# Kernel optimization log

Hardware: AMD Instinct MI355X
Metric: run time of the kernel (lower is better)

The kernel has to match this reference:

```python
import jax, jax.numpy as jnp
import numpy as np

EPS_LOG = 1e-20
EPS_DENOM = 1e-6
TEMP = 0.07  # temperature init; module uses exp(log(1/temp)) = 1/temp


def _log(t):
    return jnp.log(t + EPS_LOG)


def _masked_mean(t, mask, axis):
    t = jnp.where(mask, t, 0.0)
    numer = t.sum(axis=axis)
    denom = jnp.maximum(mask.sum(axis=axis).astype(t.dtype), EPS_DENOM)
    return numer / denom


def setup_inputs() -> dict:
    key = jax.random.key(0)
    k1, k2 = jax.random.split(key)
    B, T, I, D = 64, 64, 196, 512
    vision = jax.random.normal(k1, (B, I, D), dtype=jnp.float32)
    text = jax.random.normal(k2, (B, T, D), dtype=jnp.float32)
    # L2-normalize (as produced upstream in FILIP/CLIP) to keep exp(sim/temp) stable
    vision = vision / jnp.linalg.norm(vision, axis=-1, keepdims=True)
    text = text / jnp.linalg.norm(text, axis=-1, keepdims=True)
    vision_mask = jnp.ones((B, I), dtype=bool)
    text_mask = jnp.ones((B, T), dtype=bool)
    return {"vision": vision, "text": text, "vision_mask": vision_mask, "text_mask": text_mask}


def reference(vision, text, vision_mask, text_mask):
    temp = jnp.exp(jnp.log(jnp.asarray(1.0 / TEMP, dtype=text.dtype)))
    neg = -jnp.finfo(text.dtype).max
    # sim[x, y, t, i] = <text[x, t], vision[y, i]> * temp
    sim = jnp.einsum('xtd,yid->xyti', text, vision) * temp
    # text -> image: max over image tokens i (invalid patches masked out)
    t2i = jnp.where(vision_mask[None, :, None, :], sim, neg).max(axis=-1)  # [x, y, t]
    t2i = _masked_mean(t2i, text_mask[:, None, :], axis=-1)                # [x, y]
    # image -> text: max over text tokens t (invalid tokens masked out)
    i2t = jnp.where(text_mask[:, None, :, None], sim, neg).max(axis=-2)    # [x, y, i]
    i2t = _masked_mean(i2t, vision_mask[None, :, :], axis=-1)              # [x, y]
    t2i_exp = jnp.exp(t2i)
    i2t_exp = jnp.exp(i2t)
    t2i_pos = jnp.diagonal(t2i_exp)
    i2t_pos = jnp.diagonal(i2t_exp)
    t2i_denom = t2i_exp.sum(axis=-1)
    i2t_denom = i2t_exp.sum(axis=0)
    t2i_loss = (-_log(t2i_pos) + _log(t2i_denom)).mean(axis=-1)
    i2t_loss = (-_log(i2t_pos) + _log(i2t_denom)).mean(axis=-1)
    filip_loss = (t2i_loss + i2t_loss) / 2
    return (filip_loss, t2i_loss, i2t_loss)
```

## Files before the change

### kernel.cpp

```cpp
#include <hip/hip_runtime.h>
#include <cstdint>
#include <cstddef>

#define BATCH   64
#define TTOK    64
#define ITOK    196
#define NPAD    224
#define DDIM    512
#define BK      64
#define NTILE   (DDIM/BK)
#define XPB     4
#define MROWS   (XPB*TTOK)
#define TEMPINV 14.285714285714286f
#define EPS_LOG 1e-20f

typedef __bf16 bf16x8 __attribute__((ext_vector_type(8)));
typedef float  floatx4 __attribute__((ext_vector_type(4)));
typedef unsigned short ushort8 __attribute__((ext_vector_type(8)));

__device__ __forceinline__ void async_load16(const void* g, void* l) {
  __builtin_amdgcn_global_load_lds(
      (const __attribute__((address_space(1))) void*)g,
      (__attribute__((address_space(3))) void*)l, 16, 0, 0);
}

__device__ __forceinline__ unsigned short f2bf(float f) {
  unsigned int u = __float_as_uint(f);
  u += 0x7fffu + ((u >> 16) & 1u);
  return (unsigned short)(u >> 16);
}

#define NV_PAD (64*224*512)
#define NT_ALL (64*64*512)

__global__ void convert_kernel(const float* __restrict__ vis,
                               const float* __restrict__ txt,
                               unsigned short* __restrict__ visb,
                               unsigned short* __restrict__ txtb) {
  int t = blockIdx.x * 256 + threadIdx.x;
  int e = t * 8;
  if (e < NV_PAD) {
    int img = e / (NPAD * DDIM);
    int rem = e - img * (NPAD * DDIM);
    int row = rem >> 9;
    int d   = rem & 511;
    ushort8 o;
    if (row < ITOK) {
      const float4* src = (const float4*)(vis + ((size_t)img * ITOK + row) * DDIM + d);
      float4 a = src[0];
      float4 b = src[1];
      o[0] = f2bf(a.x); o[1] = f2bf(a.y); o[2] = f2bf(a.z); o[3] = f2bf(a.w);
      o[4] = f2bf(b.x); o[5] = f2bf(b.y); o[6] = f2bf(b.z); o[7] = f2bf(b.w);
    } else {
      o = (ushort8){0, 0, 0, 0, 0, 0, 0, 0};
    }
    *(ushort8*)(visb + e) = o;
  } else {
    int j = e - NV_PAD;
    const float4* src = (const float4*)(txt + j);
    float4 a = src[0];
    float4 b = src[1];
    ushort8 o;
    o[0] = f2bf(a.x); o[1] = f2bf(a.y); o[2] = f2bf(a.z); o[3] = f2bf(a.w);
    o[4] = f2bf(b.x); o[5] = f2bf(b.y); o[6] = f2bf(b.z); o[7] = f2bf(b.w);
    *(ushort8*)(txtb + j) = o;
  }
}

__global__ __launch_bounds__(512, 1) void filip_gemm(
    const unsigned short* __restrict__ txtb,
    const unsigned short* __restrict__ visb,
    float* __restrict__ T2I,
    float* __restrict__ I2T)
{
  __shared__ unsigned short As[2][MROWS * BK];
  __shared__ unsigned short Bs[2][NPAD * BK];
  __shared__ float t2i_part[MROWS][2];
  __shared__ float i2t_part[XPB][NPAD];

  const int tid  = threadIdx.x;
  const int lane = tid & 63;
  const int wave = tid >> 6;
  const int wm   = wave >> 1;
  const int wn   = wave & 1;
  const int lrow = lane & 15;
  const int lq   = lane >> 4;

  const int orig = blockIdx.x;
  const int xcd  = orig & 7;
  const int idx  = orig >> 3;
  const int y    = xcd * 8 + (idx & 7);
  const int xg   = idx >> 3;

  const unsigned short* tbase = txtb + (size_t)(xg * XPB) * (TTOK * DDIM);
  const unsigned short* vbase = visb + (size_t)y * (NPAD * DDIM);

  int aoff[4], boff[4];
#pragma unroll
  for (int r = 0; r < 4; ++r) {
    int s = r * 512 + tid;
    int row = s >> 3;
    int cg = (s & 7) ^ (row & 7);
    aoff[r] = row * DDIM + cg * 8;
  }
#pragma unroll
  for (int r = 0; r < 3; ++r) {
    int s = r * 512 + tid;
    int row = s >> 3;
    int cg = (s & 7) ^ (row & 7);
    boff[r] = row * DDIM + cg * 8;
  }
  {
    int s = 1536 + tid;
    int row = s >> 3;
    int cg = (s & 7) ^ (row & 7);
    boff[3] = (tid < 256) ? row * DDIM + cg * 8 : 0;
  }

  int bro0[7], bro1[7];
#pragma unroll
  for (int nt = 0; nt < 7; ++nt) {
    int row = wn * 112 + nt * 16 + lrow;
    bro0[nt] = row * BK + ((0 + lq) ^ (row & 7)) * 8;
    bro1[nt] = row * BK + ((4 + lq) ^ (row & 7)) * 8;
  }
  int aro0[4], aro1[4];
#pragma unroll
  for (int mt = 0; mt < 4; ++mt) {
    int row = wm * 64 + mt * 16 + lrow;
    aro0[mt] = row * BK + ((0 + lq) ^ (row & 7)) * 8;
    aro1[mt] = row * BK + ((4 + lq) ^ (row & 7)) * 8;
  }

  floatx4 acc[4][7];
#pragma unroll
  for (int mt = 0; mt < 4; ++mt)
#pragma unroll
    for (int nt = 0; nt < 7; ++nt)
      acc[mt][nt] = (floatx4){0.f, 0.f, 0.f, 0.f};

  {
#pragma unroll
    for (int r = 0; r < 4; ++r)
      async_load16(tbase + aoff[r], &As[0][(r * 512 + tid) * 8]);
#pragma unroll
    for (int r = 0; r < 3; ++r)
      async_load16(vbase + boff[r], &Bs[0][(r * 512 + tid) * 8]);
    if (tid < 256)
      async_load16(vbase + boff[3], &Bs[0][(1536 + tid) * 8]);
  }
  asm volatile("s_waitcnt vmcnt(0)" ::: "memory");
  __builtin_amdgcn_s_barrier();

  for (int t = 0; t < NTILE; ++t) {
    const int cur = t & 1;
    const int nxt = cur ^ 1;
    const int k1 = (t + 1) * BK;
    const bool pf = (t + 1 < NTILE);
    const unsigned short* Ac = &As[cur][0];
    const unsigned short* Bc = &Bs[cur][0];
    unsigned short* An = &As[nxt][0];
    unsigned short* Bn = &Bs[nxt][0];

    bf16x8 b0[7], b1[7], a00, a01, a02, a03, a10, a11, a12, a13;

    if (pf) {
      async_load16(tbase + aoff[0] + k1, An + (0 * 512 + tid) * 8);
      async_load16(tbase + aoff[1] + k1, An + (1 * 512 + tid) * 8);
      async_load16(tbase + aoff[2] + k1, An + (2 * 512 + tid) * 8);
    }
#pragma unroll
    for (int nt = 0; nt < 7; ++nt) b0[nt] = *(const bf16x8*)(Bc + bro0[nt]);
    a00 = *(const bf16x8*)(Ac + aro0[0]);
    a01 = *(const bf16x8*)(Ac + aro0[1]);
    __builtin_amdgcn_s_barrier();
    asm volatile("s_waitcnt lgkmcnt(0)" ::: "memory");
    __builtin_amdgcn_sched_barrier(0);
    __builtin_amdgcn_s_setprio(1);
#pragma unroll
    for (int nt = 0; nt < 7; ++nt) {
      acc[0][nt] = __builtin_amdgcn_mfma_f32_16x16x32_bf16(a00, b0[nt], acc[0][nt], 0, 0, 0);
      acc[1][nt] = __builtin_amdgcn_mfma_f32_16x16x32_bf16(a01, b0[nt], acc[1][nt], 0, 0, 0);
    }
    __builtin_amdgcn_s_setprio(0);
    __builtin_amdgcn_s_barrier();

    if (pf) {
      async_load16(tbase + aoff[3] + k1, An + (3 * 512 + tid) * 8);
      async_load16(vbase + boff[0] + k1, Bn + (0 * 512 + tid) * 8);
      async_load16(vbase + boff[1] + k1, Bn + (1 * 512 + tid) * 8);
    }
    a02 = *(const bf16x8*)(Ac + aro0[2]);
    a03 = *(const bf16x8*)(Ac + aro0[3]);
    __builtin_amdgcn_s_barrier();
    asm volatile("s_waitcnt lgkmcnt(0)" ::: "memory");
    __builtin_amdgcn_sched_barrier(0);
    __builtin_amdgcn_s_setprio(1);
#pragma unroll
    for (int nt = 0; nt < 7; ++nt) {
      acc[2][nt] = __builtin_amdgcn_mfma_f32_16x16x32_bf16(a02, b0[nt], acc[2][nt], 0, 0, 0);
      acc[3][nt] = __builtin_amdgcn_mfma_f32_16x16x32_bf16(a03, b0[nt], acc[3][nt], 0, 0, 0);
    }
    __builtin_amdgcn_s_setprio(0);
    __builtin_amdgcn_s_barrier();

    if (pf) {
      async_load16(vbase + boff[2] + k1, Bn + (2 * 512 + tid) * 8);
      if (tid < 256)
        async_load16(vbase + boff[3] + k1, Bn + (1536 + tid) * 8);
    }
#pragma unroll
    for (int nt = 0; nt < 7; ++nt) b1[nt] = *(const bf16x8*)(Bc + bro1[nt]);
    a10 = *(const bf16x8*)(Ac + aro1[0]);
    a11 = *(const bf16x8*)(Ac + aro1[1]);
    __builtin_amdgcn_s_barrier();
    asm volatile("s_waitcnt lgkmcnt(0)" ::: "memory");
    __builtin_amdgcn_sched_barrier(0);
    __builtin_amdgcn_s_setprio(1);
#pragma unroll
    for (int nt = 0; nt < 7; ++nt) {
      acc[0][nt] = __builtin_amdgcn_mfma_f32_16x16x32_bf16(a10, b1[nt], acc[0][nt], 0, 0, 0);
      acc[1][nt] = __builtin_amdgcn_mfma_f32_16x16x32_bf16(a11, b1[nt], acc[1][nt], 0, 0, 0);
    }
    __builtin_amdgcn_s_setprio(0);
    __builtin_amdgcn_s_barrier();

    a12 = *(const bf16x8*)(Ac + aro1[2]);
    a13 = *(const bf16x8*)(Ac + aro1[3]);
    __builtin_amdgcn_s_barrier();
    asm volatile("s_waitcnt lgkmcnt(0)" ::: "memory");
    __builtin_amdgcn_sched_barrier(0);
    __builtin_amdgcn_s_setprio(1);
#pragma unroll
    for (int nt = 0; nt < 7; ++nt) {
      acc[2][nt] = __builtin_amdgcn_mfma_f32_16x16x32_bf16(a12, b1[nt], acc[2][nt], 0, 0, 0);
      acc[3][nt] = __builtin_amdgcn_mfma_f32_16x16x32_bf16(a13, b1[nt], acc[3][nt], 0, 0, 0);
    }
    __builtin_amdgcn_s_setprio(0);
    asm volatile("s_waitcnt vmcnt(0)" ::: "memory");
    __builtin_amdgcn_s_barrier();
  }

#pragma unroll
  for (int mt = 0; mt < 4; ++mt) {
    float rm[4] = {-1e30f, -1e30f, -1e30f, -1e30f};
#pragma unroll
    for (int nt = 0; nt < 7; ++nt) {
      int col = wn * 112 + nt * 16 + lrow;
      if (col < ITOK) {
#pragma unroll
        for (int j = 0; j < 4; ++j) rm[j] = fmaxf(rm[j], acc[mt][nt][j]);
      }
    }
#pragma unroll
    for (int off = 1; off < 16; off <<= 1) {
#pragma unroll
      for (int j = 0; j < 4; ++j) rm[j] = fmaxf(rm[j], __shfl_xor(rm[j], off, 64));
    }
    if (lrow == 0) {
#pragma unroll
      for (int j = 0; j < 4; ++j)
        t2i_part[wm * 64 + mt * 16 + lq * 4 + j][wn] = rm[j];
    }
  }

#pragma unroll
  for (int nt = 0; nt < 7; ++nt) {
    float cm = -1e30f;
#pragma unroll
    for (int mt = 0; mt < 4; ++mt)
#pragma unroll
      for (int j = 0; j < 4; ++j) cm = fmaxf(cm, acc[mt][nt][j]);
    cm = fmaxf(cm, __shfl_xor(cm, 16, 64));
    cm = fmaxf(cm, __shfl_xor(cm, 32, 64));
    if (lq == 0) i2t_part[wm][wn * 112 + nt * 16 + lrow] = cm;
  }
  __syncthreads();

  if (wave < XPB) {
    const int p = wave;
    float ts = fmaxf(t2i_part[p * 64 + lane][0], t2i_part[p * 64 + lane][1]);
#pragma unroll
    for (int off = 32; off; off >>= 1) ts += __shfl_xor(ts, off, 64);
    float is = 0.f;
    for (int c = lane; c < ITOK; c += 64)
      is += i2t_part[p][c];
#pragma unroll
    for (int off = 32; off; off >>= 1) is += __shfl_xor(is, off, 64);
    if (lane == 0) {
      int o = (xg * XPB + p) * BATCH + y;
      T2I[o] = TEMPINV * ts * (1.0f / TTOK);
      I2T[o] = TEMPINV * is * (1.0f / ITOK);
    }
  }
}

__global__ void finalize_kernel(const float* __restrict__ T2I,
                                const float* __restrict__ I2T,
                                float* __restrict__ out) {
  int lane = threadIdx.x;
  float td = 0.f, idn = 0.f;
  for (int y = 0; y < BATCH; ++y) td  += expf(T2I[lane * BATCH + y]);
  for (int xx = 0; xx < BATCH; ++xx) idn += expf(I2T[xx * BATCH + lane]);
  float tpos = expf(T2I[lane * (BATCH + 1)]);
  float ipos = expf(I2T[lane * (BATCH + 1)]);
  float tl = -logf(tpos + EPS_LOG) + logf(td + EPS_LOG);
  float il = -logf(ipos + EPS_LOG) + logf(idn + EPS_LOG);
#pragma unroll
  for (int off = 32; off; off >>= 1) {
    tl += __shfl_xor(tl, off, 64);
    il += __shfl_xor(il, off, 64);
  }
  if (lane == 0) {
    float t2i_loss = tl * (1.0f / BATCH);
    float i2t_loss = il * (1.0f / BATCH);
    out[0] = 0.5f * (t2i_loss + i2t_loss);
    out[1] = t2i_loss;
    out[2] = i2t_loss;
  }
}

extern "C" void kernel_launch(void* const* d_in, const int* in_sizes, int n_in,
                              void* d_out, int out_size, void* d_ws, size_t ws_size,
                              hipStream_t stream) {
  const float* vis = (const float*)d_in[0];
  const float* txt = (const float*)d_in[1];
  float* out = (float*)d_out;

  char* ws = (char*)d_ws;
  unsigned short* visb = (unsigned short*)ws;
  unsigned short* txtb = (unsigned short*)(ws + (size_t)NV_PAD * 2);
  float* T2I = (float*)(ws + (size_t)(NV_PAD + NT_ALL) * 2);
  float* I2T = T2I + BATCH * BATCH;

  convert_kernel<<<(NV_PAD + NT_ALL) / 8 / 256, 256, 0, stream>>>(vis, txt, visb, txtb);
  filip_gemm<<<(BATCH / XPB) * BATCH, 512, 0, stream>>>(txtb, visb, T2I, I2T);
  finalize_kernel<<<1, 64, 0, stream>>>(T2I, I2T, out);
}
```

Before: 158.7 us.

## Split K tiles into half-stages with finer-grained async prefetch and waits

Restructures the GEMM staging so each 64-wide K tile is split into two 32-wide halves with separate LDS buffers. Prefetches are issued per half, and partial vmcnt waits let compute on the first half start before the second half lands. Vision padding grows to 256 rows so A and B share one uniform load pattern, which adds conversion and memory traffic for the padded rows. The finalize kernel is also parallelized across 256 threads, and the convert kernel's image indexing now uses shifts.

Result: faster. 153.5 us (-3.2%).

```diff
diff --git a/kernel.cpp b/kernel.cpp
--- a/kernel.cpp
+++ b/kernel.cpp
@@ -6,6 +6,7 @@
 #define TTOK    64
 #define ITOK    196
 #define NPAD    224
+#define VROWS   256
 #define DDIM    512
 #define BK      64
 #define NTILE   (DDIM/BK)
@@ -30,7 +31,7 @@
   return (unsigned short)(u >> 16);
 }
 
-#define NV_PAD (64*224*512)
+#define NV_PAD (64*VROWS*512)
 #define NT_ALL (64*64*512)
 
 __global__ void convert_kernel(const float* __restrict__ vis,
@@ -40,8 +41,8 @@
   int t = blockIdx.x * 256 + threadIdx.x;
   int e = t * 8;
   if (e < NV_PAD) {
-    int img = e / (NPAD * DDIM);
-    int rem = e - img * (NPAD * DDIM);
+    int img = e >> 17;
+    int rem = e & 131071;
     int row = rem >> 9;
     int d   = rem & 511;
     ushort8 o;
@@ -73,8 +74,8 @@
     float* __restrict__ T2I,
     float* __restrict__ I2T)
 {
-  __shared__ unsigned short As[2][MROWS * BK];
-  __shared__ unsigned short Bs[2][NPAD * BK];
+  __shared__ unsigned short As[2][2][VROWS * 32];
+  __shared__ unsigned short Bs[2][2][VROWS * 32];
   __shared__ float t2i_part[MROWS][2];
   __shared__ float i2t_part[XPB][NPAD];
 
@@ -93,43 +94,29 @@
   const int xg   = idx >> 3;
 
   const unsigned short* tbase = txtb + (size_t)(xg * XPB) * (TTOK * DDIM);
-  const unsigned short* vbase = visb + (size_t)y * (NPAD * DDIM);
-
-  int aoff[4], boff[4];
-#pragma unroll
-  for (int r = 0; r < 4; ++r) {
-    int s = r * 512 + tid;
-    int row = s >> 3;
-    int cg = (s & 7) ^ (row & 7);
-    aoff[r] = row * DDIM + cg * 8;
-  }
-#pragma unroll
-  for (int r = 0; r < 3; ++r) {
-    int s = r * 512 + tid;
-    int row = s >> 3;
-    int cg = (s & 7) ^ (row & 7);
-    boff[r] = row * DDIM + cg * 8;
-  }
-  {
-    int s = 1536 + tid;
-    int row = s >> 3;
-    int cg = (s & 7) ^ (row & 7);
-    boff[3] = (tid < 256) ? row * DDIM + cg * 8 : 0;
-  }
-
-  int bro0[7], bro1[7];
+  const unsigned short* vbase = visb + (size_t)y * (VROWS * DDIM);
+
+  int qoff[2];
+#pragma unroll
+  for (int r = 0; r < 2; ++r) {
+    int s  = r * 512 + tid;
+    int r2 = s >> 3;
+    int cg = (s & 7) ^ (r2 & 7);
+    qoff[r] = (2 * r2 + (cg >> 2)) * DDIM + (cg & 3) * 8;
+  }
+
+  int aro[4], bro[7];
+#pragma unroll
+  for (int mt = 0; mt < 4; ++mt) {
+    int row = wm * 64 + mt * 16 + lrow;
+    int r2  = row >> 1;
+    aro[mt] = r2 * 64 + (((((row & 1) << 2) + lq) ^ (r2 & 7)) << 3);
+  }
 #pragma unroll
   for (int nt = 0; nt < 7; ++nt) {
     int row = wn * 112 + nt * 16 + lrow;
-    bro0[nt] = row * BK + ((0 + lq) ^ (row & 7)) * 8;
-    bro1[nt] = row * BK + ((4 + lq) ^ (row & 7)) * 8;
-  }
-  int aro0[4], aro1[4];
-#pragma unroll
-  for (int mt = 0; mt < 4; ++mt) {
-    int row = wm * 64 + mt * 16 + lrow;
-    aro0[mt] = row * BK + ((0 + lq) ^ (row & 7)) * 8;
-    aro1[mt] = row * BK + ((4 + lq) ^ (row & 7)) * 8;
+    int r2  = row >> 1;
+    bro[nt] = r2 * 64 + (((((row & 1) << 2) + lq) ^ (r2 & 7)) << 3);
   }
 
   floatx4 acc[4][7];
@@ -139,17 +126,20 @@
     for (int nt = 0; nt < 7; ++nt)
       acc[mt][nt] = (floatx4){0.f, 0.f, 0.f, 0.f};
 
-  {
-#pragma unroll
-    for (int r = 0; r < 4; ++r)
-      async_load16(tbase + aoff[r], &As[0][(r * 512 + tid) * 8]);
-#pragma unroll
-    for (int r = 0; r < 3; ++r)
-      async_load16(vbase + boff[r], &Bs[0][(r * 512 + tid) * 8]);
-    if (tid < 256)
-      async_load16(vbase + boff[3], &Bs[0][(1536 + tid) * 8]);
-  }
-  asm volatile("s_waitcnt vmcnt(0)" ::: "memory");
+  auto stageAh = [&](int b, int h, int kbase) {
+    async_load16(tbase + qoff[0] + kbase, &As[b][h][(0 * 512 + tid) * 8]);
+    async_load16(tbase + qoff[1] + kbase, &As[b][h][(1 * 512 + tid) * 8]);
+  };
+  auto stageBh = [&](int b, int h, int kbase) {
+    async_load16(vbase + qoff[0] + kbase, &Bs[b][h][(0 * 512 + tid) * 8]);
+    async_load16(vbase + qoff[1] + kbase, &Bs[b][h][(1 * 512 + tid) * 8]);
+  };
+
+  stageAh(0, 0, 0);
+  stageBh(0, 0, 0);
+  stageAh(0, 1, 32);
+  stageBh(0, 1, 32);
+  asm volatile("s_waitcnt vmcnt(4)" ::: "memory");
   __builtin_amdgcn_s_barrier();
 
   for (int t = 0; t < NTILE; ++t) {
@@ -157,87 +147,78 @@
     const int nxt = cur ^ 1;
     const int k1 = (t + 1) * BK;
     const bool pf = (t + 1 < NTILE);
-    const unsigned short* Ac = &As[cur][0];
-    const unsigned short* Bc = &Bs[cur][0];
-    unsigned short* An = &As[nxt][0];
-    unsigned short* Bn = &Bs[nxt][0];
-
-    bf16x8 b0[7], b1[7], a00, a01, a02, a03, a10, a11, a12, a13;
-
-    if (pf) {
-      async_load16(tbase + aoff[0] + k1, An + (0 * 512 + tid) * 8);
-      async_load16(tbase + aoff[1] + k1, An + (1 * 512 + tid) * 8);
-      async_load16(tbase + aoff[2] + k1, An + (2 * 512 + tid) * 8);
-    }
-#pragma unroll
-    for (int nt = 0; nt < 7; ++nt) b0[nt] = *(const bf16x8*)(Bc + bro0[nt]);
-    a00 = *(const bf16x8*)(Ac + aro0[0]);
-    a01 = *(const bf16x8*)(Ac + aro0[1]);
+    const unsigned short* Ac0 = &As[cur][0][0];
+    const unsigned short* Ac1 = &As[cur][1][0];
+    const unsigned short* Bc0 = &Bs[cur][0][0];
+    const unsigned short* Bc1 = &Bs[cur][1][0];
+
+    bf16x8 b0[7], b1[7], x0, x1;
+
+#pragma unroll
+    for (int nt = 0; nt < 7; ++nt) b0[nt] = *(const bf16x8*)(Bc0 + bro[nt]);
+    x0 = *(const bf16x8*)(Ac0 + aro[0]);
+    x1 = *(const bf16x8*)(Ac0 + aro[1]);
+    if (pf) stageAh(nxt, 0, k1);
     __builtin_amdgcn_s_barrier();
     asm volatile("s_waitcnt lgkmcnt(0)" ::: "memory");
     __builtin_amdgcn_sched_barrier(0);
     __builtin_amdgcn_s_setprio(1);
 #pragma unroll
     for (int nt = 0; nt < 7; ++nt) {
-      acc[0][nt] = __builtin_amdgcn_mfma_f32_16x16x32_bf16(a00, b0[nt], acc[0][nt], 0, 0, 0);
-      acc[1][nt] = __builtin_amdgcn_mfma_f32_16x16x32_bf16(a01, b0[nt], acc[1][nt], 0, 0, 0);
+      acc[0][nt] = __builtin_amdgcn_mfma_f32_16x16x32_bf16(x0, b0[nt], acc[0][nt], 0, 0, 0);
+      acc[1][nt] = __builtin_amdgcn_mfma_f32_16x16x32_bf16(x1, b0[nt], acc[1][nt], 0, 0, 0);
     }
     __builtin_amdgcn_s_setprio(0);
     __builtin_amdgcn_s_barrier();
 
-    if (pf) {
-      async_load16(tbase + aoff[3] + k1, An + (3 * 512 + tid) * 8);
-      async_load16(vbase + boff[0] + k1, Bn + (0 * 512 + tid) * 8);
-      async_load16(vbase + boff[1] + k1, Bn + (1 * 512 + tid) * 8);
-    }
-    a02 = *(const bf16x8*)(Ac + aro0[2]);
-    a03 = *(const bf16x8*)(Ac + aro0[3]);
+    x0 = *(const bf16x8*)(Ac0 + aro[2]);
+    x1 = *(const bf16x8*)(Ac0 + aro[3]);
+    if (pf) stageBh(nxt, 0, k1);
     __builtin_amdgcn_s_barrier();
     asm volatile("s_waitcnt lgkmcnt(0)" ::: "memory");
     __builtin_amdgcn_sched_barrier(0);
     __builtin_amdgcn_s_setprio(1);
 #pragma unroll
     for (int nt = 0; nt < 7; ++nt) {
-      acc[2][nt] = __builtin_amdgcn_mfma_f32_16x16x32_bf16(a02, b0[nt], acc[2][nt], 0, 0, 0);
-      acc[3][nt] = __builtin_amdgcn_mfma_f32_16x16x32_bf16(a03, b0[nt], acc[3][nt], 0, 0, 0);
+      acc[2][nt] = __builtin_amdgcn_mfma_f32_16x16x32_bf16(x0, b0[nt], acc[2][nt], 0, 0, 0);
+      acc[3][nt] = __builtin_amdgcn_mfma_f32_16x16x32_bf16(x1, b0[nt], acc[3][nt], 0, 0, 0);
     }
     __builtin_amdgcn_s_setprio(0);
-    __builtin_amdgcn_s_barrier();
-
-    if (pf) {
-      async_load16(vbase + boff[2] + k1, Bn + (2 * 512 + tid) * 8);
-      if (tid < 256)
-        async_load16(vbase + boff[3] + k1, Bn + (1536 + tid) * 8);
-    }
-#pragma unroll
-    for (int nt = 0; nt < 7; ++nt) b1[nt] = *(const bf16x8*)(Bc + bro1[nt]);
-    a10 = *(const bf16x8*)(Ac + aro1[0]);
-    a11 = *(const bf16x8*)(Ac + aro1[1]);
+    if (t == NTILE - 1) { asm volatile("s_waitcnt vmcnt(0)" ::: "memory"); }
+    else                { asm volatile("s_waitcnt vmcnt(4)" ::: "memory"); }
+    __builtin_amdgcn_s_barrier();
+
+#pragma unroll
+    for (int nt = 0; nt < 7; ++nt) b1[nt] = *(const bf16x8*)(Bc1 + bro[nt]);
+    x0 = *(const bf16x8*)(Ac1 + aro[0]);
+    x1 = *(const bf16x8*)(Ac1 + aro[1]);
+    if (pf) stageAh(nxt, 1, k1 + 32);
     __builtin_amdgcn_s_barrier();
     asm volatile("s_waitcnt lgkmcnt(0)" ::: "memory");
     __builtin_amdgcn_sched_barrier(0);
     __builtin_amdgcn_s_setprio(1);
 #pragma unroll
     for (int nt = 0; nt < 7; ++nt) {
-      acc[0][nt] = __builtin_amdgcn_mfma_f32_16x16x32_bf16(a10, b1[nt], acc[0][nt], 0, 0, 0);
-      acc[1][nt] = __builtin_amdgcn_mfma_f32_16x16x32_bf16(a11, b1[nt], acc[1][nt], 0, 0, 0);
+      acc[0][nt] = __builtin_amdgcn_mfma_f32_16x16x32_bf16(x0, b1[nt], acc[0][nt], 0, 0, 0);
+      acc[1][nt] = __builtin_amdgcn_mfma_f32_16x16x32_bf16(x1, b1[nt], acc[1][nt], 0, 0, 0);
     }
     __builtin_amdgcn_s_setprio(0);
     __builtin_amdgcn_s_barrier();
 
-    a12 = *(const bf16x8*)(Ac + aro1[2]);
-    a13 = *(const bf16x8*)(Ac + aro1[3]);
+    x0 = *(const bf16x8*)(Ac1 + aro[2]);
+    x1 = *(const bf16x8*)(Ac1 + aro[3]);
+    if (pf) stageBh(nxt, 1, k1 + 32);
     __builtin_amdgcn_s_barrier();
     asm volatile("s_waitcnt lgkmcnt(0)" ::: "memory");
     __builtin_amdgcn_sched_barrier(0);
     __builtin_amdgcn_s_setprio(1);
 #pragma unroll
     for (int nt = 0; nt < 7; ++nt) {
-      acc[2][nt] = __builtin_amdgcn_mfma_f32_16x16x32_bf16(a12, b1[nt], acc[2][nt], 0, 0, 0);
-      acc[3][nt] = __builtin_amdgcn_mfma_f32_16x16x32_bf16(a13, b1[nt], acc[3][nt], 0, 0, 0);
+      acc[2][nt] = __builtin_amdgcn_mfma_f32_16x16x32_bf16(x0, b1[nt], acc[2][nt], 0, 0, 0);
+      acc[3][nt] = __builtin_amdgcn_mfma_f32_16x16x32_bf16(x1, b1[nt], acc[3][nt], 0, 0, 0);
     }
     __builtin_amdgcn_s_setprio(0);
-    asm volatile("s_waitcnt vmcnt(0)" ::: "memory");
+    if (pf) { asm volatile("s_waitcnt vmcnt(4)" ::: "memory"); }
     __builtin_amdgcn_s_barrier();
   }
 
@@ -298,25 +279,44 @@
 __global__ void finalize_kernel(const float* __restrict__ T2I,
                                 const float* __restrict__ I2T,
                                 float* __restrict__ out) {
-  int lane = threadIdx.x;
-  float td = 0.f, idn = 0.f;
-  for (int y = 0; y < BATCH; ++y) td  += expf(T2I[lane * BATCH + y]);
-  for (int xx = 0; xx < BATCH; ++xx) idn += expf(I2T[xx * BATCH + lane]);
-  float tpos = expf(T2I[lane * (BATCH + 1)]);
-  float ipos = expf(I2T[lane * (BATCH + 1)]);
-  float tl = -logf(tpos + EPS_LOG) + logf(td + EPS_LOG);
-  float il = -logf(ipos + EPS_LOG) + logf(idn + EPS_LOG);
-#pragma unroll
-  for (int off = 32; off; off >>= 1) {
-    tl += __shfl_xor(tl, off, 64);
-    il += __shfl_xor(il, off, 64);
-  }
-  if (lane == 0) {
-    float t2i_loss = tl * (1.0f / BATCH);
-    float i2t_loss = il * (1.0f / BATCH);
-    out[0] = 0.5f * (t2i_loss + i2t_loss);
-    out[1] = t2i_loss;
-    out[2] = i2t_loss;
+  __shared__ float tl_s[64], il_s[64];
+  int tid = threadIdx.x;
+  int r = tid >> 2, q = tid & 3;
+  float td = 0.f;
+  const float4* rp = (const float4*)(T2I + r * 64 + q * 16);
+#pragma unroll
+  for (int i = 0; i < 4; ++i) {
+    float4 v = rp[i];
+    td += expf(v.x) + expf(v.y) + expf(v.z) + expf(v.w);
+  }
+  td += __shfl_xor(td, 1, 64);
+  td += __shfl_xor(td, 2, 64);
+  float idn = 0.f;
+#pragma unroll
+  for (int i = 0; i < 16; ++i) idn += expf(I2T[(q * 16 + i) * 64 + r]);
+  idn += __shfl_xor(idn, 1, 64);
+  idn += __shfl_xor(idn, 2, 64);
+  if (q == 0) {
+    float tpos = expf(T2I[r * 65]);
+    float ipos = expf(I2T[r * 65]);
+    tl_s[r] = -logf(tpos + EPS_LOG) + logf(td + EPS_LOG);
+    il_s[r] = -logf(ipos + EPS_LOG) + logf(idn + EPS_LOG);
+  }
+  __syncthreads();
+  if (tid < 64) {
+    float tl = tl_s[tid], il = il_s[tid];
+#pragma unroll
+    for (int off = 32; off; off >>= 1) {
+      tl += __shfl_xor(tl, off, 64);
+      il += __shfl_xor(il, off, 64);
+    }
+    if (tid == 0) {
+      float t2i_loss = tl * (1.0f / BATCH);
+      float i2t_loss = il * (1.0f / BATCH);
+      out[0] = 0.5f * (t2i_loss + i2t_loss);
+      out[1] = t2i_loss;
+      out[2] = i2t_loss;
+    }
   }
 }
 
@@ -335,5 +335,5 @@
 
   convert_kernel<<<(NV_PAD + NT_ALL) / 8 / 256, 256, 0, stream>>>(vis, txt, visb, txtb);
   filip_gemm<<<(BATCH / XPB) * BATCH, 512, 0, stream>>>(txtb, visb, T2I, I2T);
-  finalize_kernel<<<1, 64, 0, stream>>>(T2I, I2T, out);
-}
+  finalize_kernel<<<1, 256, 0, stream>>>(T2I, I2T, out);
+}
```
